# Optimization experiments

Measured on AMD Instinct MI355X. Metric: run time of the kernel, lower is better.

Reference implementation:

```python
import jax, jax.numpy as jnp
import numpy as np

PHI_C = 0.9
ALPHA = 0.9
EPS = 1e-06
K_MAX = 100


def setup_inputs() -> dict:
    key = jax.random.key(0)
    k1, k2, k3 = jax.random.split(key, 3)
    B, D_IN, D_H, D_OUT = 16384, 1024, 4096, 1024
    x = jax.random.normal(k1, (B, D_IN), dtype=jnp.float32)
    W1 = jax.random.normal(k2, (D_IN, D_H), dtype=jnp.float32) * 0.02
    b1 = jnp.zeros((D_H,), dtype=jnp.float32)
    W2 = jax.random.normal(k3, (D_H, D_OUT), dtype=jnp.float32) * 0.02
    b2 = jnp.zeros((D_OUT,), dtype=jnp.float32)
    return {"x": x, "W1": W1, "b1": b1, "W2": W2, "b2": b2}


def _base_net(x, W1, b1, W2, b2):
    h = jax.nn.relu(x @ W1 + b1)
    return h @ W2 + b2  # [B, D_OUT]


def _fixed_point(out):
    # y_{k+1} = y_k + alpha * phi_c * tanh(out - y_k), with early exit when
    # max|y_{k+1} - y_k| < eps (the converging step IS applied, as in torch).
    y0 = jnp.zeros_like(out)

    def step(carry, _):
        y, done = carry
        y_next = y + ALPHA * PHI_C * jnp.tanh(out - y)
        converged = jnp.max(jnp.abs(y_next - y)) < EPS
        y_new = jnp.where(done, y, y_next)
        return (y_new, done | converged), None

    (y, _), _ = jax.lax.scan(step, (y0, jnp.array(False)), None, length=K_MAX)
    return y


def reference(x, W1, b1, W2, b2):
    out = _base_net(x, W1, b1, W2, b2)
    return _fixed_point(out)
```

## Files before the change

### kernel.cpp

```cpp
#include <hip/hip_runtime.h>
#include <hip/hip_bf16.h>
#include <stdint.h>


#define DEV __device__ __forceinline__

typedef short bf16x8 __attribute__((ext_vector_type(8)));
typedef float f32x4 __attribute__((ext_vector_type(4)));

typedef __attribute__((address_space(1))) const unsigned char* gptr1_t;
typedef __attribute__((address_space(3))) unsigned char* lptr3_t;

DEV void async_copy16(const void* g, void* l) {
  __builtin_amdgcn_global_load_lds((gptr1_t)g, (lptr3_t)l, 16, 0, 0);
}

DEV unsigned short f2bf(float f) {
  union { float f; unsigned u; } v; v.f = f;
  unsigned u = v.u + 0x7FFFu + ((v.u >> 16) & 1u);
  return (unsigned short)(u >> 16);
}

#define BAR()   __builtin_amdgcn_s_barrier()
#define LGKM0() asm volatile("s_waitcnt lgkmcnt(0)" ::: "memory")
#define VMW(n)  asm volatile("s_waitcnt vmcnt(" #n ")" ::: "memory")


__global__ void cvt_f32_bf16(const float4* __restrict__ in,
                             ushort4* __restrict__ out, int n4) {
  int i = blockIdx.x * blockDim.x + threadIdx.x;
  if (i >= n4) return;
  float4 v = in[i];
  ushort4 o;
  o.x = f2bf(v.x); o.y = f2bf(v.y); o.z = f2bf(v.z); o.w = f2bf(v.w);
  out[i] = o;
}

__global__ void transpose_f32_bf16(const float* __restrict__ in,
                                   unsigned short* __restrict__ out,
                                   int R, int C) {
  __shared__ float tile[32][33];
  int c0 = blockIdx.x * 32, r0 = blockIdx.y * 32;
  int tx = threadIdx.x, ty = threadIdx.y;
#pragma unroll
  for (int i = 0; i < 32; i += 8)
    tile[ty + i][tx] = in[(long)(r0 + ty + i) * C + (c0 + tx)];
  __syncthreads();
#pragma unroll
  for (int i = 0; i < 32; i += 8)
    out[(long)(c0 + ty + i) * R + (r0 + tx)] = f2bf(tile[tx][ty + i]);
}


#define LDA(base, m, ks) \
  (*(const bf16x8*)((base) + abase + (m) * 2048 + (c0 ^ ((ks) << 6))))
#define LDB(base, n, ks) \
  (*(const bf16x8*)((base) + bbase + (n) * 2048 + (c0 ^ ((ks) << 6))))

#define RD_A(dst, base, m0_)                                   \
  _Pragma("unroll") for (int m_ = 0; m_ < 4; ++m_) {           \
    dst[m_][0] = LDA(base, (m0_) + m_, 0);                     \
    dst[m_][1] = LDA(base, (m0_) + m_, 1);                     \
  }
#define RD_B(dst, base, n0_)                                   \
  _Pragma("unroll") for (int n_ = 0; n_ < 2; ++n_) {           \
    dst[n_][0] = LDB(base, (n0_) + n_, 0);                     \
    dst[n_][1] = LDB(base, (n0_) + n_, 1);                     \
  }

#define QUAD(MB, NB, AF, BF)                                                \
  do {                                                                      \
    __builtin_amdgcn_s_setprio(1);                                          \
    _Pragma("unroll") for (int m_ = 0; m_ < 4; ++m_)                        \
    _Pragma("unroll") for (int n_ = 0; n_ < 2; ++n_) {                      \
      acc[(MB) + m_][(NB) + n_] = __builtin_amdgcn_mfma_f32_16x16x32_bf16(  \
          AF[m_][0], BF[n_][0], acc[(MB) + m_][(NB) + n_], 0, 0, 0);        \
      acc[(MB) + m_][(NB) + n_] = __builtin_amdgcn_mfma_f32_16x16x32_bf16(  \
          AF[m_][1], BF[n_][1], acc[(MB) + m_][(NB) + n_], 0, 0, 0);        \
    }                                                                       \
    __builtin_amdgcn_s_setprio(0);                                          \
  } while (0)

#define ST_A_LO(dstw, koff) { async_copy16(gA[0] + (koff), (dstw));          \
                              async_copy16(gA[2] + (koff), (dstw) + 16384); }
#define ST_A_HI(dstw, koff) { async_copy16(gA[1] + (koff), (dstw) + 8192);   \
                              async_copy16(gA[3] + (koff), (dstw) + 24576); }
#define ST_B_LO(dstw, koff) { async_copy16(gB[0] + (koff), (dstw));          \
                              async_copy16(gB[1] + (koff), (dstw) + 8192); }
#define ST_B_HI(dstw, koff) { async_copy16(gB[2] + (koff), (dstw) + 16384);  \
                              async_copy16(gB[3] + (koff), (dstw) + 24576); }

template <bool RELU_BF16>
__global__ __launch_bounds__(512, 2)
void gemm256(const unsigned short* __restrict__ A,
             const unsigned short* __restrict__ BT,
             const float* __restrict__ bias,
             void* __restrict__ Cout,
             int M, int N, int K, int nbn_shift) {
  extern __shared__ char lds[];
  const char* aE = lds;
  const char* aO = lds + 32768;
  const char* bE = lds + 65536;
  const char* bO = lds + 98304;

  const int tid = threadIdx.x;
  const int wave = tid >> 6, lane = tid & 63;
  const int wr = wave >> 2, wc = wave & 3;

  char* aEw = (char*)aE + wave * 1024;
  char* aOw = (char*)aO + wave * 1024;
  char* bEw = (char*)bE + wave * 1024;
  char* bOw = (char*)bO + wave * 1024;

  const int nwg = gridDim.x;
  const int wg = blockIdx.x;
  const int swz = (wg & 7) * (nwg >> 3) + (wg >> 3);
  const int bm = swz >> nbn_shift;
  const int bn = swz & ((1 << nbn_shift) - 1);
  const int m0 = bm << 8, n0 = bn << 8;

  const int srow = tid >> 3;
  const int sk = ((tid & 7) ^ (srow & 7)) << 3;
  const unsigned short* gA[4];
  const unsigned short* gB[4];
#pragma unroll
  for (int c = 0; c < 4; ++c) {
    gA[c] = A + (size_t)(m0 + c * 64 + srow) * K + sk;
    gB[c] = BT + (size_t)(n0 + c * 64 + srow) * K + sk;
  }

  const int lr = lane & 15, lg = lane >> 4;
  const int c0 = ((lg ^ (lr & 7)) << 4);
  const int abase = (wr * 128 + lr) * 128;
  const int bbase = (wc * 64 + lr) * 128;

  f32x4 acc[8][4] = {};
  bf16x8 af[4][2], b01[2][2], b23[2][2];

  ST_B_LO(bEw, 0);  ST_B_HI(bEw, 0);
  ST_A_LO(aEw, 0);  ST_A_HI(aEw, 0);
  ST_B_LO(bOw, 64); ST_B_HI(bOw, 64);
  VMW(6);
  BAR();

  const int NT = K >> 6;
  const int nIt = NT >> 1;

  for (int it = 0; it < nIt - 1; ++it) {
    const int kO  = (2 * it + 1) << 6;
    const int kE2 = (2 * it + 2) << 6;
    const int kO2 = (2 * it + 3) << 6;
    RD_A(af, aE, 0); RD_B(b01, bE, 0); ST_A_LO(aOw, kO);
    BAR(); LGKM0(); QUAD(0, 0, af, b01); BAR();
    RD_B(b23, bE, 2); ST_A_HI(aOw, kO);
    BAR(); LGKM0(); QUAD(0, 2, af, b23); VMW(8); BAR();
    RD_A(af, aE, 4); ST_B_LO(bEw, kE2);
    BAR(); LGKM0(); QUAD(4, 2, af, b23); BAR();
    ST_B_HI(bEw, kE2);
    BAR(); QUAD(4, 0, af, b01); VMW(6); BAR();
    RD_A(af, aO, 0); RD_B(b01, bO, 0); ST_A_LO(aEw, kE2);
    BAR(); LGKM0(); QUAD(0, 0, af, b01); BAR();
    RD_B(b23, bO, 2); ST_A_HI(aEw, kE2);
    BAR(); LGKM0(); QUAD(0, 2, af, b23); VMW(8); BAR();
    RD_A(af, aO, 4); ST_B_LO(bOw, kO2);
    BAR(); LGKM0(); QUAD(4, 2, af, b23); BAR();
    ST_B_HI(bOw, kO2);
    BAR(); QUAD(4, 0, af, b01); VMW(6); BAR();
  }

  {
    const int kO = (NT - 1) << 6;
    RD_A(af, aE, 0); RD_B(b01, bE, 0); ST_A_LO(aOw, kO);
    BAR(); LGKM0(); QUAD(0, 0, af, b01); BAR();
    RD_B(b23, bE, 2); ST_A_HI(aOw, kO);
    BAR(); LGKM0(); QUAD(0, 2, af, b23); VMW(8); BAR();
    RD_A(af, aE, 4);
    BAR(); LGKM0(); QUAD(4, 2, af, b23); BAR();
    BAR(); QUAD(4, 0, af, b01); VMW(2); BAR();
    RD_A(af, aO, 0); RD_B(b01, bO, 0);
    BAR(); LGKM0(); QUAD(0, 0, af, b01); BAR();
    RD_B(b23, bO, 2);
    BAR(); LGKM0(); QUAD(0, 2, af, b23); VMW(0); BAR();
    RD_A(af, aO, 4);
    BAR(); LGKM0(); QUAD(4, 2, af, b23); BAR();
    QUAD(4, 0, af, b01);
  }

  const int ccol = n0 + wc * 64;
  const int crow = m0 + wr * 128;
  float bv[4];
#pragma unroll
  for (int n = 0; n < 4; ++n) bv[n] = bias[ccol + n * 16 + lr];

  if (RELU_BF16) {
    unsigned short* O = (unsigned short*)Cout;
#pragma unroll
    for (int m = 0; m < 8; ++m)
#pragma unroll
      for (int j = 0; j < 4; ++j) {
        size_t r = (size_t)(crow + m * 16 + lg * 4 + j) * N;
#pragma unroll
        for (int n = 0; n < 4; ++n) {
          float v = acc[m][n][j] + bv[n];
          O[r + ccol + n * 16 + lr] = f2bf(fmaxf(v, 0.0f));
        }
      }
  } else {
    float* O = (float*)Cout;
#pragma unroll
    for (int m = 0; m < 8; ++m)
#pragma unroll
      for (int j = 0; j < 4; ++j) {
        size_t r = (size_t)(crow + m * 16 + lg * 4 + j) * N;
#pragma unroll
        for (int n = 0; n < 4; ++n)
          O[r + ccol + n * 16 + lr] = acc[m][n][j] + bv[n];
      }
  }
}


extern "C" void kernel_launch(void* const* d_in, const int* in_sizes, int n_in,
                              void* d_out, int out_size, void* d_ws,
                              size_t ws_size, hipStream_t stream) {
  const float* x  = (const float*)d_in[0];
  const float* W1 = (const float*)d_in[1];
  const float* b1 = (const float*)d_in[2];
  const float* W2 = (const float*)d_in[3];
  const float* b2 = (const float*)d_in[4];
  float* out = (float*)d_out;

  const int B = 16384, DIN = 1024, DH = 4096, DOUT = 1024;

  size_t need = (size_t)B * DIN * 2 + (size_t)DIN * DH * 2 +
                (size_t)DH * DOUT * 2 + (size_t)B * DH * 2;
  if (ws_size < need) return;

  char* ws = (char*)d_ws;
  unsigned short* xb  = (unsigned short*)ws;  ws += (size_t)B * DIN * 2;
  unsigned short* w1t = (unsigned short*)ws;  ws += (size_t)DIN * DH * 2;
  unsigned short* w2t = (unsigned short*)ws;  ws += (size_t)DH * DOUT * 2;
  unsigned short* h   = (unsigned short*)ws;

  hipFuncSetAttribute((const void*)gemm256<true>,
                      hipFuncAttributeMaxDynamicSharedMemorySize, 131072);
  hipFuncSetAttribute((const void*)gemm256<false>,
                      hipFuncAttributeMaxDynamicSharedMemorySize, 131072);

  int n4 = B * DIN / 4;
  cvt_f32_bf16<<<n4 / 256, 256, 0, stream>>>((const float4*)x, (ushort4*)xb, n4);
  transpose_f32_bf16<<<dim3(DH / 32, DIN / 32), dim3(32, 8), 0, stream>>>(W1, w1t, DIN, DH);
  transpose_f32_bf16<<<dim3(DOUT / 32, DH / 32), dim3(32, 8), 0, stream>>>(W2, w2t, DH, DOUT);

  gemm256<true><<<dim3((B / 256) * (DH / 256)), 512, 131072, stream>>>(
      xb, w1t, b1, h, B, DH, DIN, 4);
  gemm256<false><<<dim3((B / 256) * (DOUT / 256)), 512, 131072, stream>>>(
      h, w2t, b2, out, B, DOUT, DH, 2);
}
```

Baseline: 280.4 us.

## Restructure GEMM LDS layout into half-tiles and refill sub-buffers eagerly

The GEMM kernel's LDS tile layout changes so each A and B buffer is split into two halves, and the rows a wave reads are remapped to match. The ping-pong schedule is rewritten so each half-tile is refilled with the next K-step as soon as its fragments are consumed, instead of refilling whole buffers. This keeps more global-to-LDS copies in flight and removes some wait points, aiming to hide load latency better. The barrier and waitcnt sequencing is subtle, so correctness and actual overlap depend on the exact counts used. The epilogue mapping of waves to output rows and columns appears unchanged, which may not match the new fragment-to-row assignment.

```diff
diff --git a/kernel.cpp b/kernel.cpp
--- a/kernel.cpp
+++ b/kernel.cpp
@@ -52,21 +52,28 @@
 }
 
 
-#define LDA(base, m, ks) \
-  (*(const bf16x8*)((base) + abase + (m) * 2048 + (c0 ^ ((ks) << 6))))
-#define LDB(base, n, ks) \
-  (*(const bf16x8*)((base) + bbase + (n) * 2048 + (c0 ^ ((ks) << 6))))
-
-#define RD_A(dst, base, m0_)                                   \
-  _Pragma("unroll") for (int m_ = 0; m_ < 4; ++m_) {           \
-    dst[m_][0] = LDA(base, (m0_) + m_, 0);                     \
-    dst[m_][1] = LDA(base, (m0_) + m_, 1);                     \
-  }
-#define RD_B(dst, base, n0_)                                   \
-  _Pragma("unroll") for (int n_ = 0; n_ < 2; ++n_) {           \
-    dst[n_][0] = LDB(base, (n0_) + n_, 0);                     \
-    dst[n_][1] = LDB(base, (n0_) + n_, 1);                     \
-  }
+#define RD_AFL(dst, bufA)                                                     \
+  _Pragma("unroll") for (int m_ = 0; m_ < 4; ++m_)                            \
+  _Pragma("unroll") for (int k_ = 0; k_ < 2; ++k_)                            \
+    dst[m_][k_] = *(const bf16x8*)((bufA) + (wr * 64 + m_ * 16 + lr) * 128 +  \
+                                   (c0 ^ (k_ << 6)));
+#define RD_AFH(dst, bufA)                                                     \
+  _Pragma("unroll") for (int m_ = 0; m_ < 4; ++m_)                            \
+  _Pragma("unroll") for (int k_ = 0; k_ < 2; ++k_)                            \
+    dst[m_][k_] = *(const bf16x8*)((bufA) + 16384 +                           \
+                                   (wr * 64 + m_ * 16 + lr) * 128 +           \
+                                   (c0 ^ (k_ << 6)));
+#define RD_B01(dst, bufB)                                                     \
+  _Pragma("unroll") for (int n_ = 0; n_ < 2; ++n_)                            \
+  _Pragma("unroll") for (int k_ = 0; k_ < 2; ++k_)                            \
+    dst[n_][k_] = *(const bf16x8*)((bufB) + (wc * 32 + n_ * 16 + lr) * 128 +  \
+                                   (c0 ^ (k_ << 6)));
+#define RD_B23(dst, bufB)                                                     \
+  _Pragma("unroll") for (int n_ = 0; n_ < 2; ++n_)                            \
+  _Pragma("unroll") for (int k_ = 0; k_ < 2; ++k_)                            \
+    dst[n_][k_] = *(const bf16x8*)((bufB) + 16384 +                           \
+                                   (wc * 32 + n_ * 16 + lr) * 128 +           \
+                                   (c0 ^ (k_ << 6)));
 
 #define QUAD(MB, NB, AF, BF)                                                \
   do {                                                                      \
@@ -81,36 +88,36 @@
     __builtin_amdgcn_s_setprio(0);                                          \
   } while (0)
 
-#define ST_A_LO(dstw, koff) { async_copy16(gA[0] + (koff), (dstw));          \
-                              async_copy16(gA[2] + (koff), (dstw) + 16384); }
-#define ST_A_HI(dstw, koff) { async_copy16(gA[1] + (koff), (dstw) + 8192);   \
-                              async_copy16(gA[3] + (koff), (dstw) + 24576); }
-#define ST_B_LO(dstw, koff) { async_copy16(gB[0] + (koff), (dstw));          \
-                              async_copy16(gB[1] + (koff), (dstw) + 8192); }
-#define ST_B_HI(dstw, koff) { async_copy16(gB[2] + (koff), (dstw) + 16384);  \
-                              async_copy16(gB[3] + (koff), (dstw) + 24576); }
+#define SA_LO(bufw, koff) { async_copy16(gAlo0 + (koff), (bufw));            \
+                            async_copy16(gAlo1 + (koff), (bufw) + 8192); }
+#define SA_HI(bufw, koff) { async_copy16(gAhi0 + (koff), (bufw) + 16384);    \
+                            async_copy16(gAhi1 + (koff), (bufw) + 24576); }
+#define SB_01(bufw, koff) { async_copy16(gB010 + (koff), (bufw));            \
+                            async_copy16(gB011 + (koff), (bufw) + 8192); }
+#define SB_23(bufw, koff) { async_copy16(gB230 + (koff), (bufw) + 16384);    \
+                            async_copy16(gB231 + (koff), (bufw) + 24576); }
 
 template <bool RELU_BF16>
 __global__ __launch_bounds__(512, 2)
-void gemm256(const unsigned short* __restrict__ A,
-             const unsigned short* __restrict__ BT,
-             const float* __restrict__ bias,
-             void* __restrict__ Cout,
-             int M, int N, int K, int nbn_shift) {
+void gemm8p(const unsigned short* __restrict__ A,
+            const unsigned short* __restrict__ BT,
+            const float* __restrict__ bias,
+            void* __restrict__ Cout,
+            int M, int N, int K, int nbn_shift) {
   extern __shared__ char lds[];
-  const char* aE = lds;
-  const char* aO = lds + 32768;
-  const char* bE = lds + 65536;
-  const char* bO = lds + 98304;
+  char* Ap = lds;
+  char* Aq = lds + 32768;
+  char* Bp = lds + 65536;
+  char* Bq = lds + 98304;
 
   const int tid = threadIdx.x;
   const int wave = tid >> 6, lane = tid & 63;
   const int wr = wave >> 2, wc = wave & 3;
 
-  char* aEw = (char*)aE + wave * 1024;
-  char* aOw = (char*)aO + wave * 1024;
-  char* bEw = (char*)bE + wave * 1024;
-  char* bOw = (char*)bO + wave * 1024;
+  char* Apw = Ap + wave * 1024;
+  char* Aqw = Aq + wave * 1024;
+  char* Bpw = Bp + wave * 1024;
+  char* Bqw = Bq + wave * 1024;
 
   const int nwg = gridDim.x;
   const int wg = blockIdx.x;
@@ -119,69 +126,66 @@
   const int bn = swz & ((1 << nbn_shift) - 1);
   const int m0 = bm << 8, n0 = bn << 8;
 
-  const int srow = tid >> 3;
-  const int sk = ((tid & 7) ^ (srow & 7)) << 3;
-  const unsigned short* gA[4];
-  const unsigned short* gB[4];
-#pragma unroll
-  for (int c = 0; c < 4; ++c) {
-    gA[c] = A + (size_t)(m0 + c * 64 + srow) * K + sk;
-    gB[c] = BT + (size_t)(n0 + c * 64 + srow) * K + sk;
-  }
+  const int rho = tid >> 3;
+  const int sk = ((tid & 7) ^ (rho & 7)) << 3;
+  const unsigned short* gAlo0 = A + (size_t)(m0 + rho) * K + sk;
+  const unsigned short* gAlo1 = A + (size_t)(m0 + 128 + rho) * K + sk;
+  const unsigned short* gAhi0 = gAlo0 + (size_t)64 * K;
+  const unsigned short* gAhi1 = gAlo1 + (size_t)64 * K;
+  const int bgr = ((rho >> 5) << 6) + (rho & 31);
+  const unsigned short* gB010 = BT + (size_t)(n0 + bgr) * K + sk;
+  const unsigned short* gB011 = BT + (size_t)(n0 + 128 + bgr) * K + sk;
+  const unsigned short* gB230 = gB010 + (size_t)32 * K;
+  const unsigned short* gB231 = gB011 + (size_t)32 * K;
 
   const int lr = lane & 15, lg = lane >> 4;
   const int c0 = ((lg ^ (lr & 7)) << 4);
-  const int abase = (wr * 128 + lr) * 128;
-  const int bbase = (wc * 64 + lr) * 128;
 
   f32x4 acc[8][4] = {};
   bf16x8 af[4][2], b01[2][2], b23[2][2];
 
-  ST_B_LO(bEw, 0);  ST_B_HI(bEw, 0);
-  ST_A_LO(aEw, 0);  ST_A_HI(aEw, 0);
-  ST_B_LO(bOw, 64); ST_B_HI(bOw, 64);
+  SA_LO(Apw, 0); SA_HI(Apw, 0); SB_01(Bpw, 0); SB_23(Bpw, 0);
+  SA_LO(Aqw, 64); SB_01(Bqw, 64); SB_23(Bqw, 64);
   VMW(6);
   BAR();
 
   const int NT = K >> 6;
-  const int nIt = NT >> 1;
-
-  for (int it = 0; it < nIt - 1; ++it) {
-    const int kO  = (2 * it + 1) << 6;
-    const int kE2 = (2 * it + 2) << 6;
-    const int kO2 = (2 * it + 3) << 6;
-    RD_A(af, aE, 0); RD_B(b01, bE, 0); ST_A_LO(aOw, kO);
-    BAR(); LGKM0(); QUAD(0, 0, af, b01); BAR();
-    RD_B(b23, bE, 2); ST_A_HI(aOw, kO);
-    BAR(); LGKM0(); QUAD(0, 2, af, b23); VMW(8); BAR();
-    RD_A(af, aE, 4); ST_B_LO(bEw, kE2);
-    BAR(); LGKM0(); QUAD(4, 2, af, b23); BAR();
-    ST_B_HI(bEw, kE2);
+
+  for (int it = 0; it < (NT - 2) / 2; ++it) {
+    const int t = 2 * it;
+    const int k1 = (t + 1) << 6, k2 = (t + 2) << 6, k3 = (t + 3) << 6;
+    RD_AFL(af, Ap); RD_B01(b01, Bp); SA_HI(Aqw, k1);
+    BAR(); LGKM0(); QUAD(0, 0, af, b01); BAR();
+    RD_B23(b23, Bp); SA_LO(Apw, k2);
+    BAR(); LGKM0(); QUAD(0, 2, af, b23); BAR();
+    RD_AFH(af, Ap); SB_01(Bpw, k2);
+    BAR(); LGKM0(); QUAD(4, 2, af, b23); BAR();
+    SB_23(Bpw, k2);
     BAR(); QUAD(4, 0, af, b01); VMW(6); BAR();
-    RD_A(af, aO, 0); RD_B(b01, bO, 0); ST_A_LO(aEw, kE2);
-    BAR(); LGKM0(); QUAD(0, 0, af, b01); BAR();
-    RD_B(b23, bO, 2); ST_A_HI(aEw, kE2);
-    BAR(); LGKM0(); QUAD(0, 2, af, b23); VMW(8); BAR();
-    RD_A(af, aO, 4); ST_B_LO(bOw, kO2);
-    BAR(); LGKM0(); QUAD(4, 2, af, b23); BAR();
-    ST_B_HI(bOw, kO2);
+    RD_AFL(af, Aq); RD_B01(b01, Bq); SA_HI(Apw, k2);
+    BAR(); LGKM0(); QUAD(0, 0, af, b01); BAR();
+    RD_B23(b23, Bq); SA_LO(Aqw, k3);
+    BAR(); LGKM0(); QUAD(0, 2, af, b23); BAR();
+    RD_AFH(af, Aq); SB_01(Bqw, k3);
+    BAR(); LGKM0(); QUAD(4, 2, af, b23); BAR();
+    SB_23(Bqw, k3);
     BAR(); QUAD(4, 0, af, b01); VMW(6); BAR();
   }
 
   {
-    const int kO = (NT - 1) << 6;
-    RD_A(af, aE, 0); RD_B(b01, bE, 0); ST_A_LO(aOw, kO);
-    BAR(); LGKM0(); QUAD(0, 0, af, b01); BAR();
-    RD_B(b23, bE, 2); ST_A_HI(aOw, kO);
-    BAR(); LGKM0(); QUAD(0, 2, af, b23); VMW(8); BAR();
-    RD_A(af, aE, 4);
-    BAR(); LGKM0(); QUAD(4, 2, af, b23); BAR();
-    BAR(); QUAD(4, 0, af, b01); VMW(2); BAR();
-    RD_A(af, aO, 0); RD_B(b01, bO, 0);
-    BAR(); LGKM0(); QUAD(0, 0, af, b01); BAR();
-    RD_B(b23, bO, 2);
-    BAR(); LGKM0(); QUAD(0, 2, af, b23); VMW(0); BAR();
-    RD_A(af, aO, 4);
+    const int kL = (NT - 1) << 6;
+    RD_AFL(af, Ap); RD_B01(b01, Bp); SA_HI(Aqw, kL);
+    BAR(); LGKM0(); QUAD(0, 0, af, b01); BAR();
+    RD_B23(b23, Bp);
+    BAR(); LGKM0(); QUAD(0, 2, af, b23); BAR();
+    RD_AFH(af, Ap);
+    BAR(); LGKM0(); QUAD(4, 2, af, b23); BAR();
+    BAR(); QUAD(4, 0, af, b01); VMW(0); BAR();
+    RD_AFL(af, Aq); RD_B01(b01, Bq);
+    BAR(); LGKM0(); QUAD(0, 0, af, b01); BAR();
+    RD_B23(b23, Bq);
+    BAR(); LGKM0(); QUAD(0, 2, af, b23); BAR();
+    RD_AFH(af, Aq);
     BAR(); LGKM0(); QUAD(4, 2, af, b23); BAR();
     QUAD(4, 0, af, b01);
   }
@@ -242,9 +246,9 @@
   unsigned short* w2t = (unsigned short*)ws;  ws += (size_t)DH * DOUT * 2;
   unsigned short* h   = (unsigned short*)ws;
 
-  hipFuncSetAttribute((const void*)gemm256<true>,
+  hipFuncSetAttribute((const void*)gemm8p<true>,
                       hipFuncAttributeMaxDynamicSharedMemorySize, 131072);
-  hipFuncSetAttribute((const void*)gemm256<false>,
+  hipFuncSetAttribute((const void*)gemm8p<false>,
                       hipFuncAttributeMaxDynamicSharedMemorySize, 131072);
 
   int n4 = B * DIN / 4;
@@ -252,8 +256,8 @@
   transpose_f32_bf16<<<dim3(DH / 32, DIN / 32), dim3(32, 8), 0, stream>>>(W1, w1t, DIN, DH);
   transpose_f32_bf16<<<dim3(DOUT / 32, DH / 32), dim3(32, 8), 0, stream>>>(W2, w2t, DH, DOUT);
 
-  gemm256<true><<<dim3((B / 256) * (DH / 256)), 512, 131072, stream>>>(
+  gemm8p<true><<<dim3((B / 256) * (DH / 256)), 512, 131072, stream>>>(
       xb, w1t, b1, h, B, DH, DIN, 4);
-  gemm256<false><<<dim3((B / 256) * (DOUT / 256)), 512, 131072, stream>>>(
+  gemm8p<false><<<dim3((B / 256) * (DOUT / 256)), 512, 131072, stream>>>(
       h, w2t, b2, out, B, DOUT, DH, 2);
 }
```

Measured after the change: 284.2 us. About the same (+1.4%).
